# Performance work log

Hardware: AMD Instinct MI355X
Metric: run time of the kernel (lower is better)

The kernel has to match this reference:

```python
import jax, jax.numpy as jnp
import numpy as np

B, N = 8192, 2048


def setup_inputs() -> dict:
    key = jax.random.key(0)
    k1, k2 = jax.random.split(key)
    predictions = jax.random.normal(k1, (B, N), dtype=jnp.float32)
    targets = jax.random.normal(k2, (B, N), dtype=jnp.float32)
    return {"predictions": predictions, "targets": targets}


def reference(predictions, targets):
    # Original: per-batch NxN squared-difference cost matrix + scipy Hungarian,
    # then MSE(pred, optimally-permuted targets), averaged over the batch.
    # For scalar entries with cost (p_i - t_j)^2 the optimal assignment is the
    # monotone matching (rearrangement inequality): sort both vectors and pair
    # in order. This computes the exact same loss, fully vectorized.
    p_sorted = jnp.sort(predictions, axis=-1)  # [B, N]
    t_sorted = jnp.sort(targets, axis=-1)      # [B, N]
    # mean over N per row, then mean over B == global mean
    return jnp.mean((p_sorted - t_sorted) ** 2)
```

## Files before the change

### kernel.cpp

```cpp
#include <hip/hip_runtime.h>
#include <math.h>

#define ROWS 8192
#define NCOL 2048
#define V 32
#define WPB 4
#define THREADS (WPB * 64)

__device__ __forceinline__ void ce(float& a, float& b) {
  const float lo = fminf(a, b);
  const float hi = fmaxf(a, b);
  a = lo; b = hi;
}

__device__ __forceinline__ float ce_dir(float a, float b, float cdir) {
  return __builtin_amdgcn_fmed3f(a, b, cdir);
}

__global__ __launch_bounds__(THREADS, 4) void sort_mse_kernel(
    const float* __restrict__ pred, const float* __restrict__ targ,
    float* __restrict__ out) {
  const int lane = threadIdx.x & 63;
  const int wave = threadIdx.x >> 6;
  const int row = blockIdx.x * WPB + wave;
  const size_t base = (size_t)row * NCOL + (size_t)lane * V;

  float rp[V], rt[V];
  const float4* p4 = (const float4*)(pred + base);
  const float4* t4 = (const float4*)(targ + base);
#pragma unroll
  for (int q = 0; q < V / 4; ++q) {
    const float4 a = p4[q];
    rp[4 * q + 0] = a.x; rp[4 * q + 1] = a.y;
    rp[4 * q + 2] = a.z; rp[4 * q + 3] = a.w;
    const float4 b = t4[q];
    rt[4 * q + 0] = b.x; rt[4 * q + 1] = b.y;
    rt[4 * q + 2] = b.z; rt[4 * q + 3] = b.w;
  }

#pragma unroll
  for (int k = 2; k <= V; k <<= 1) {
#pragma unroll
    for (int v = 0; v < V; ++v) {
      if ((v & (k >> 1)) == 0) {
        ce(rp[v], rp[v ^ (k - 1)]);
        ce(rt[v], rt[v ^ (k - 1)]);
      }
    }
#pragma unroll
    for (int j = k >> 2; j >= 1; j >>= 1) {
#pragma unroll
      for (int v = 0; v < V; ++v) {
        if ((v & j) == 0) {
          ce(rp[v], rp[v | j]);
          ce(rt[v], rt[v | j]);
        }
      }
    }
  }

  for (int kb = 1; kb <= 32; kb <<= 1) {
    {
      const int lm = 2 * kb - 1;
      const float cdir = (lane & kb) ? INFINITY : -INFINITY;
#pragma unroll
      for (int q = 0; q < 4; ++q) {
        const int vA = 4 * q;
        float o[8];
#pragma unroll
        for (int u = 0; u < 4; ++u) {
          o[u]     = __shfl_xor(rp[(vA + u) ^ 31], lm, 64);
          o[u + 4] = __shfl_xor(rp[vA + u], lm, 64);
        }
#pragma unroll
        for (int u = 0; u < 4; ++u) {
          rp[vA + u]        = ce_dir(rp[vA + u],        o[u],     cdir);
          rp[(vA + u) ^ 31] = ce_dir(rp[(vA + u) ^ 31], o[u + 4], cdir);
        }
#pragma unroll
        for (int u = 0; u < 4; ++u) {
          o[u]     = __shfl_xor(rt[(vA + u) ^ 31], lm, 64);
          o[u + 4] = __shfl_xor(rt[vA + u], lm, 64);
        }
#pragma unroll
        for (int u = 0; u < 4; ++u) {
          rt[vA + u]        = ce_dir(rt[vA + u],        o[u],     cdir);
          rt[(vA + u) ^ 31] = ce_dir(rt[(vA + u) ^ 31], o[u + 4], cdir);
        }
      }
    }
    for (int m = kb >> 1; m >= 1; m >>= 1) {
      const float cdir = (lane & m) ? INFINITY : -INFINITY;
#pragma unroll
      for (int c = 0; c < V; c += 8) {
        float o[8];
#pragma unroll
        for (int u = 0; u < 8; ++u) o[u] = __shfl_xor(rp[c + u], m, 64);
#pragma unroll
        for (int u = 0; u < 8; ++u) rp[c + u] = ce_dir(rp[c + u], o[u], cdir);
#pragma unroll
        for (int u = 0; u < 8; ++u) o[u] = __shfl_xor(rt[c + u], m, 64);
#pragma unroll
        for (int u = 0; u < 8; ++u) rt[c + u] = ce_dir(rt[c + u], o[u], cdir);
      }
    }
#pragma unroll
    for (int j = 16; j >= 1; j >>= 1) {
#pragma unroll
      for (int v = 0; v < V; ++v) {
        if ((v & j) == 0) {
          ce(rp[v], rp[v | j]);
          ce(rt[v], rt[v | j]);
        }
      }
    }
  }

  float acc = 0.f;
#pragma unroll
  for (int v = 0; v < V; ++v) {
    const float d = rp[v] - rt[v];
    acc = fmaf(d, d, acc);
  }
#pragma unroll
  for (int off = 32; off > 0; off >>= 1) acc += __shfl_down(acc, off, 64);
  if (lane == 0) {
    unsafeAtomicAdd(out, acc * (1.0f / ((float)ROWS * (float)NCOL)));
  }
}

extern "C" void kernel_launch(void* const* d_in, const int* in_sizes, int n_in,
                              void* d_out, int out_size, void* d_ws, size_t ws_size,
                              hipStream_t stream) {
  const float* pred = (const float*)d_in[0];
  const float* targ = (const float*)d_in[1];
  float* out = (float*)d_out;

  hipMemsetAsync(out, 0, sizeof(float), stream);
  sort_mse_kernel<<<ROWS / WPB, THREADS, 0, stream>>>(pred, targ, out);
}
```

Measured before the change: 244.7 us.

## Use ds_swizzle for cross-lane exchanges and sort pred/targ arrays sequentially

Replaces __shfl_xor (ds_bpermute with address computation) with ds_swizzle in XOR mode for masks up to 31, and keeps bpermute with a precomputed address only for the lane^63 case. The merge loops are fully templated, so every mask and pass count is a compile-time constant. The two arrays are now sorted one after the other instead of interleaved, and launch bounds drop from 4 to 2 blocks per SIMD. This cuts per-shuffle address overhead and loop control but gives up instruction-level interleaving between the two sorts, and may lower occupancy.

```diff
diff --git a/kernel.cpp b/kernel.cpp
--- a/kernel.cpp
+++ b/kernel.cpp
@@ -17,13 +17,97 @@
   return __builtin_amdgcn_fmed3f(a, b, cdir);
 }
 
-__global__ __launch_bounds__(THREADS, 4) void sort_mse_kernel(
+template <int M>
+__device__ __forceinline__ float lane_xor(float x, int a63) {
+  if constexpr (M == 63) {
+    return __builtin_bit_cast(
+        float, __builtin_amdgcn_ds_bpermute(a63, __builtin_bit_cast(int, x)));
+  } else {
+    static_assert(M >= 1 && M <= 31, "swizzle mask");
+    constexpr int pat = (M << 10) | 0x1F;
+    return __builtin_bit_cast(
+        float, __builtin_amdgcn_ds_swizzle(__builtin_bit_cast(int, x), pat));
+  }
+}
+
+template <int M>
+__device__ __forceinline__ void xpass1(float (&x)[V], float cdir, int a63) {
+#pragma unroll
+  for (int c = 0; c < V; c += 8) {
+    float o[8];
+#pragma unroll
+    for (int u = 0; u < 8; ++u) o[u] = lane_xor<M>(x[c + u], a63);
+#pragma unroll
+    for (int u = 0; u < 8; ++u) x[c + u] = ce_dir(x[c + u], o[u], cdir);
+  }
+}
+
+template <int KB>
+__device__ __forceinline__ void merge1(float (&x)[V], int lane, int a63) {
+  {
+    constexpr int LM = 2 * KB - 1;
+    const float cdir = (lane & KB) ? INFINITY : -INFINITY;
+#pragma unroll
+    for (int q = 0; q < 4; ++q) {
+      const int vA = 4 * q;
+      float o[8];
+#pragma unroll
+      for (int u = 0; u < 4; ++u) {
+        o[u]     = lane_xor<LM>(x[(vA + u) ^ 31], a63);
+        o[u + 4] = lane_xor<LM>(x[vA + u], a63);
+      }
+#pragma unroll
+      for (int u = 0; u < 4; ++u) {
+        x[vA + u]        = ce_dir(x[vA + u],        o[u],     cdir);
+        x[(vA + u) ^ 31] = ce_dir(x[(vA + u) ^ 31], o[u + 4], cdir);
+      }
+    }
+  }
+  if constexpr (KB >= 32) xpass1<16>(x, (lane & 16) ? INFINITY : -INFINITY, a63);
+  if constexpr (KB >= 16) xpass1<8>(x, (lane & 8) ? INFINITY : -INFINITY, a63);
+  if constexpr (KB >= 8)  xpass1<4>(x, (lane & 4) ? INFINITY : -INFINITY, a63);
+  if constexpr (KB >= 4)  xpass1<2>(x, (lane & 2) ? INFINITY : -INFINITY, a63);
+  if constexpr (KB >= 2)  xpass1<1>(x, (lane & 1) ? INFINITY : -INFINITY, a63);
+#pragma unroll
+  for (int j = 16; j >= 1; j >>= 1) {
+#pragma unroll
+    for (int v = 0; v < V; ++v) {
+      if ((v & j) == 0) ce(x[v], x[v | j]);
+    }
+  }
+}
+
+__device__ __forceinline__ void sort_one(float (&x)[V], int lane, int a63) {
+#pragma unroll
+  for (int k = 2; k <= V; k <<= 1) {
+#pragma unroll
+    for (int v = 0; v < V; ++v) {
+      if ((v & (k >> 1)) == 0) ce(x[v], x[v ^ (k - 1)]);
+    }
+#pragma unroll
+    for (int j = k >> 2; j >= 1; j >>= 1) {
+#pragma unroll
+      for (int v = 0; v < V; ++v) {
+        if ((v & j) == 0) ce(x[v], x[v | j]);
+      }
+    }
+  }
+  merge1<1>(x, lane, a63);
+  merge1<2>(x, lane, a63);
+  merge1<4>(x, lane, a63);
+  merge1<8>(x, lane, a63);
+  merge1<16>(x, lane, a63);
+  merge1<32>(x, lane, a63);
+}
+
+__global__ __launch_bounds__(THREADS, 2) void sort_mse_kernel(
     const float* __restrict__ pred, const float* __restrict__ targ,
     float* __restrict__ out) {
   const int lane = threadIdx.x & 63;
   const int wave = threadIdx.x >> 6;
   const int row = blockIdx.x * WPB + wave;
   const size_t base = (size_t)row * NCOL + (size_t)lane * V;
+  const int a63 = ((lane ^ 63) << 2);
 
   float rp[V], rt[V];
   const float4* p4 = (const float4*)(pred + base);
@@ -38,83 +122,8 @@
     rt[4 * q + 2] = b.z; rt[4 * q + 3] = b.w;
   }
 
-#pragma unroll
-  for (int k = 2; k <= V; k <<= 1) {
-#pragma unroll
-    for (int v = 0; v < V; ++v) {
-      if ((v & (k >> 1)) == 0) {
-        ce(rp[v], rp[v ^ (k - 1)]);
-        ce(rt[v], rt[v ^ (k - 1)]);
-      }
-    }
-#pragma unroll
-    for (int j = k >> 2; j >= 1; j >>= 1) {
-#pragma unroll
-      for (int v = 0; v < V; ++v) {
-        if ((v & j) == 0) {
-          ce(rp[v], rp[v | j]);
-          ce(rt[v], rt[v | j]);
-        }
-      }
-    }
-  }
-
-  for (int kb = 1; kb <= 32; kb <<= 1) {
-    {
-      const int lm = 2 * kb - 1;
-      const float cdir = (lane & kb) ? INFINITY : -INFINITY;
-#pragma unroll
-      for (int q = 0; q < 4; ++q) {
-        const int vA = 4 * q;
-        float o[8];
-#pragma unroll
-        for (int u = 0; u < 4; ++u) {
-          o[u]     = __shfl_xor(rp[(vA + u) ^ 31], lm, 64);
-          o[u + 4] = __shfl_xor(rp[vA + u], lm, 64);
-        }
-#pragma unroll
-        for (int u = 0; u < 4; ++u) {
-          rp[vA + u]        = ce_dir(rp[vA + u],        o[u],     cdir);
-          rp[(vA + u) ^ 31] = ce_dir(rp[(vA + u) ^ 31], o[u + 4], cdir);
-        }
-#pragma unroll
-        for (int u = 0; u < 4; ++u) {
-          o[u]     = __shfl_xor(rt[(vA + u) ^ 31], lm, 64);
-          o[u + 4] = __shfl_xor(rt[vA + u], lm, 64);
-        }
-#pragma unroll
-        for (int u = 0; u < 4; ++u) {
-          rt[vA + u]        = ce_dir(rt[vA + u],        o[u],     cdir);
-          rt[(vA + u) ^ 31] = ce_dir(rt[(vA + u) ^ 31], o[u + 4], cdir);
-        }
-      }
-    }
-    for (int m = kb >> 1; m >= 1; m >>= 1) {
-      const float cdir = (lane & m) ? INFINITY : -INFINITY;
-#pragma unroll
-      for (int c = 0; c < V; c += 8) {
-        float o[8];
-#pragma unroll
-        for (int u = 0; u < 8; ++u) o[u] = __shfl_xor(rp[c + u], m, 64);
-#pragma unroll
-        for (int u = 0; u < 8; ++u) rp[c + u] = ce_dir(rp[c + u], o[u], cdir);
-#pragma unroll
-        for (int u = 0; u < 8; ++u) o[u] = __shfl_xor(rt[c + u], m, 64);
-#pragma unroll
-        for (int u = 0; u < 8; ++u) rt[c + u] = ce_dir(rt[c + u], o[u], cdir);
-      }
-    }
-#pragma unroll
-    for (int j = 16; j >= 1; j >>= 1) {
-#pragma unroll
-      for (int v = 0; v < V; ++v) {
-        if ((v & j) == 0) {
-          ce(rp[v], rp[v | j]);
-          ce(rt[v], rt[v | j]);
-        }
-      }
-    }
-  }
+  sort_one(rp, lane, a63);
+  sort_one(rt, lane, a63);
 
   float acc = 0.f;
 #pragma unroll
```

Result: slower. 256.7 us (+4.9%).
